# Optimization experiments

Hardware: AMD Instinct MI355X
Metric: run time of the kernel (lower is better)

## Reference

```python
import jax, jax.numpy as jnp
import numpy as np

B, S, V = 1, 4096, 50265
D, H, DH, FF, L = 768, 12, 64, 3072, 12
W = 256  # one-sided window (longformer-base attention_window=512)
EPS = 1e-5
NEG = -1e9


def _ln(x, s, b):
    mu = jnp.mean(x, -1, keepdims=True)
    var = jnp.mean(jnp.square(x - mu), -1, keepdims=True)
    return (x - mu) * jax.lax.rsqrt(var + EPS) * s + b


def _sliding_attn(q, k, v, key_mask):
    # q,k,v: [B,H,S,DH]; key_mask: [B,S] (1 = attend). Banded attention |i-j| <= W.
    b, h, s, dh = q.shape
    c = W
    nc = s // c
    idx = jnp.arange(nc)[:, None] * c + jnp.arange(3 * c)[None, :]  # index into padded key axis
    kp = jnp.pad(k, ((0, 0), (0, 0), (c, c), (0, 0)))
    vp = jnp.pad(v, ((0, 0), (0, 0), (c, c), (0, 0)))
    k3 = kp[:, :, idx]  # [B,H,nc,3c,DH]
    v3 = vp[:, :, idx]
    qc = q.reshape(b, h, nc, c, dh)
    scores = jnp.einsum('bhncd,bhnmd->bhncm', qc, k3) * (1.0 / (dh ** 0.5))
    rel = jnp.arange(3 * c)[None, :] - c - jnp.arange(c)[:, None]  # key_pos - query_pos, [c,3c]
    band = jnp.abs(rel) <= W
    km = jnp.pad(key_mask.astype(bool), ((0, 0), (c, c)))[:, idx]  # [B,nc,3c]
    valid = band[None, None, None] & km[:, None, :, None, :]
    probs = jax.nn.softmax(jnp.where(valid, scores, NEG), axis=-1)
    out = jnp.einsum('bhncm,bhnmd->bhncd', probs, v3)
    return out.reshape(b, h, s, dh)


def _forward(input_ids, attention_mask, word_emb, pos_emb, emb_ln_s, emb_ln_b,
             Wq, bq, Wk, bk, Wv, bv, Wo, bo, ln1_s, ln1_b,
             W1, b1, W2, b2, ln2_s, ln2_b,
             h1w, h1b, h2w, h2b, h3w, h3b):
    b, s = input_ids.shape
    pos = jnp.arange(s) + 2  # roberta-style position offset (padding_idx=1)
    x = word_emb[input_ids] + pos_emb[pos][None]
    x = _ln(x, emb_ln_s, emb_ln_b)
    key_mask = attention_mask

    def block(xc, p):
        wq, bq_, wk, bk_, wv, bv_, wo, bo_, l1s, l1b, w1, b1_, w2, b2_, l2s, l2b = p
        q = (xc @ wq + bq_).reshape(b, s, H, DH).transpose(0, 2, 1, 3)
        k = (xc @ wk + bk_).reshape(b, s, H, DH).transpose(0, 2, 1, 3)
        v = (xc @ wv + bv_).reshape(b, s, H, DH).transpose(0, 2, 1, 3)
        a = _sliding_attn(q, k, v, key_mask).transpose(0, 2, 1, 3).reshape(b, s, D)
        xc = _ln(xc + a @ wo + bo_, l1s, l1b)
        hdd = jax.nn.gelu(xc @ w1 + b1_, approximate=False)
        xc = _ln(xc + hdd @ w2 + b2_, l2s, l2b)
        return xc, None

    x, _ = jax.lax.scan(block, x, (Wq, bq, Wk, bk, Wv, bv, Wo, bo,
                                   ln1_s, ln1_b, W1, b1, W2, b2, ln2_s, ln2_b))

    # gather hidden state at last occurrence of token id 2 (</s>) per row
    eq = (input_ids == 2).astype(jnp.int32)
    sep = s - 1 - jnp.argmax(eq[:, ::-1], axis=1)
    emb = x[jnp.arange(b), sep]  # [B, D]

    z = jax.nn.relu(emb @ h1w + h1b)
    z = jax.nn.relu(z @ h2w + h2b)
    return jnp.tanh(z @ h3w + h3b)  # [B, 1]


def setup_inputs() -> dict:
    key = jax.random.key(0)
    ks = jax.random.split(key, 24)
    sc = 0.02

    def n(k, shape):
        return jax.random.normal(k, shape, jnp.float32) * sc

    input_ids = jax.random.randint(ks[0], (B, S), 0, V)
    input_ids = input_ids.at[:, -1].set(2)  # guarantee a </s> token (id 2)
    attention_mask = jnp.ones((B, S), jnp.int32)
    return {
        'input_ids': input_ids,
        'attention_mask': attention_mask,
        'word_emb': n(ks[1], (V, D)),
        'pos_emb': n(ks[2], (S + 2, D)),
        'emb_ln_s': jnp.ones((D,), jnp.float32),
        'emb_ln_b': jnp.zeros((D,), jnp.float32),
        'Wq': n(ks[3], (L, D, D)), 'bq': jnp.zeros((L, D), jnp.float32),
        'Wk': n(ks[4], (L, D, D)), 'bk': jnp.zeros((L, D), jnp.float32),
        'Wv': n(ks[5], (L, D, D)), 'bv': jnp.zeros((L, D), jnp.float32),
        'Wo': n(ks[6], (L, D, D)), 'bo': jnp.zeros((L, D), jnp.float32),
        'ln1_s': jnp.ones((L, D), jnp.float32), 'ln1_b': jnp.zeros((L, D), jnp.float32),
        'W1': n(ks[7], (L, D, FF)), 'b1': jnp.zeros((L, FF), jnp.float32),
        'W2': n(ks[8], (L, FF, D)), 'b2': jnp.zeros((L, D), jnp.float32),
        'ln2_s': jnp.ones((L, D), jnp.float32), 'ln2_b': jnp.zeros((L, D), jnp.float32),
        'h1w': n(ks[9], (D, 512)), 'h1b': jnp.zeros((512,), jnp.float32),
        'h2w': n(ks[10], (512, 256)), 'h2b': jnp.zeros((256,), jnp.float32),
        'h3w': n(ks[11], (256, 1)), 'h3b': jnp.zeros((1,), jnp.float32),
    }


def reference(input_ids, attention_mask, word_emb, pos_emb, emb_ln_s, emb_ln_b,
              Wq, bq, Wk, bk, Wv, bv, Wo, bo, ln1_s, ln1_b,
              W1, b1, W2, b2, ln2_s, ln2_b,
              h1w, h1b, h2w, h2b, h3w, h3b):
    return _forward(input_ids, attention_mask, word_emb, pos_emb, emb_ln_s, emb_ln_b,
                    Wq, bq, Wk, bk, Wv, bv, Wo, bo, ln1_s, ln1_b,
                    W1, b1, W2, b2, ln2_s, ln2_b,
                    h1w, h1b, h2w, h2b, h3w, h3b)
```

## Files before the change

### kernel.cpp

```cpp
#include <hip/hip_runtime.h>
#include <math.h>

#define S_LEN 4096
#define DMODEL 768
#define NHEAD 12
#define DHEAD 64
#define FFDIM 3072
#define NLAYER 12
#define WIN 256
#define QKVN 2304

typedef __bf16 bf16x8 __attribute__((ext_vector_type(8)));
typedef unsigned short u16x8 __attribute__((ext_vector_type(8)));
typedef unsigned short u16x4 __attribute__((ext_vector_type(4)));
typedef float f32x4 __attribute__((ext_vector_type(4)));

__device__ inline unsigned short f2bf(float f) {
    unsigned int u = __float_as_uint(f);
    u += 0x7fff + ((u >> 16) & 1);
    return (unsigned short)(u >> 16);
}

__device__ inline void gload16(const void* g, void* l) {
    __builtin_amdgcn_global_load_lds((const __attribute__((address_space(1))) void*)g,
                                     (__attribute__((address_space(3))) void*)l, 16, 0, 0);
}

__global__ __launch_bounds__(256) void ln_kernel(const float* __restrict__ in,
                                                 const float* __restrict__ s,
                                                 const float* __restrict__ b,
                                                 float* __restrict__ out,
                                                 unsigned short* __restrict__ outb) {
    const int wv = threadIdx.x >> 6, lane = threadIdx.x & 63;
    const int row = blockIdx.x * 4 + wv;
    const float* p = in + (size_t)row * DMODEL;
    const int c = lane * 4;
    float4 v0 = *(const float4*)&p[c];
    float4 v1 = *(const float4*)&p[c + 256];
    float4 v2 = *(const float4*)&p[c + 512];
    float sum = v0.x + v0.y + v0.z + v0.w + v1.x + v1.y + v1.z + v1.w
              + v2.x + v2.y + v2.z + v2.w;
    float sq  = v0.x*v0.x + v0.y*v0.y + v0.z*v0.z + v0.w*v0.w
              + v1.x*v1.x + v1.y*v1.y + v1.z*v1.z + v1.w*v1.w
              + v2.x*v2.x + v2.y*v2.y + v2.z*v2.z + v2.w*v2.w;
    #pragma unroll
    for (int off = 32; off; off >>= 1) {
        sum += __shfl_xor(sum, off);
        sq  += __shfl_xor(sq, off);
    }
    const float mu = sum * (1.0f / DMODEL);
    const float var = sq * (1.0f / DMODEL) - mu * mu;
    const float rs = rsqrtf(var + 1e-5f);
    float* o = out + (size_t)row * DMODEL;
    unsigned short* ob = outb + (size_t)row * DMODEL;
    #pragma unroll
    for (int seg = 0; seg < 3; ++seg) {
        const int cc = c + seg * 256;
        float4 v = (seg == 0) ? v0 : (seg == 1) ? v1 : v2;
        float4 sv = *(const float4*)&s[cc];
        float4 bv = *(const float4*)&b[cc];
        float4 r;
        r.x = (v.x - mu) * rs * sv.x + bv.x;
        r.y = (v.y - mu) * rs * sv.y + bv.y;
        r.z = (v.z - mu) * rs * sv.z + bv.z;
        r.w = (v.w - mu) * rs * sv.w + bv.w;
        *(float4*)&o[cc] = r;
        u16x4 pk;
        pk[0] = f2bf(r.x); pk[1] = f2bf(r.y); pk[2] = f2bf(r.z); pk[3] = f2bf(r.w);
        *(u16x4*)&ob[cc] = pk;
    }
}

__device__ inline void block_reduce2(float& sum, float& sq) {
    #pragma unroll
    for (int off = 32; off; off >>= 1) {
        sum += __shfl_xor(sum, off);
        sq  += __shfl_xor(sq, off);
    }
    __shared__ float red[8];
    int wid = threadIdx.x >> 6, lane = threadIdx.x & 63;
    if (lane == 0) { red[wid] = sum; red[wid + 4] = sq; }
    __syncthreads();
    sum = red[0] + red[1] + red[2] + red[3];
    sq  = red[4] + red[5] + red[6] + red[7];
    __syncthreads();
}

__global__ __launch_bounds__(256) void embed_ln_kernel(const int* __restrict__ ids,
                                                       const float* __restrict__ wemb,
                                                       const float* __restrict__ pemb,
                                                       const float* __restrict__ s,
                                                       const float* __restrict__ b,
                                                       float* __restrict__ out,
                                                       unsigned short* __restrict__ outb) {
    int row = blockIdx.x, tid = threadIdx.x;
    int id = ids[row];
    const float* wp = wemb + (size_t)id * DMODEL;
    const float* pp = pemb + (size_t)(row + 2) * DMODEL;
    float v0 = wp[tid] + pp[tid];
    float v1 = wp[tid + 256] + pp[tid + 256];
    float v2 = wp[tid + 512] + pp[tid + 512];
    float sum = v0 + v1 + v2;
    float sq  = v0 * v0 + v1 * v1 + v2 * v2;
    block_reduce2(sum, sq);
    float mu = sum * (1.0f / DMODEL);
    float var = sq * (1.0f / DMODEL) - mu * mu;
    float rs = rsqrtf(var + 1e-5f);
    float* o = out + (size_t)row * DMODEL;
    unsigned short* ob = outb + (size_t)row * DMODEL;
    float r0 = (v0 - mu) * rs * s[tid]       + b[tid];
    float r1 = (v1 - mu) * rs * s[tid + 256] + b[tid + 256];
    float r2 = (v2 - mu) * rs * s[tid + 512] + b[tid + 512];
    o[tid] = r0; o[tid + 256] = r1; o[tid + 512] = r2;
    ob[tid] = f2bf(r0); ob[tid + 256] = f2bf(r1); ob[tid + 512] = f2bf(r2);
}

__global__ __launch_bounds__(256) void transpose_all(const float* __restrict__ wq,
                                                     const float* __restrict__ wk,
                                                     const float* __restrict__ wv,
                                                     const float* __restrict__ wo,
                                                     const float* __restrict__ w1,
                                                     const float* __restrict__ w2,
                                                     unsigned short* __restrict__ dq,
                                                     unsigned short* __restrict__ dk,
                                                     unsigned short* __restrict__ dv,
                                                     unsigned short* __restrict__ dwo,
                                                     unsigned short* __restrict__ d1,
                                                     unsigned short* __restrict__ d2) {
    const int id = blockIdx.x;
    const float* src; unsigned short* dst; int C, R, bx, by;
    if (id < 2304) {
        const int m = id / 576, t2 = id % 576;
        src = (m == 0) ? wq : (m == 1) ? wk : (m == 2) ? wv : wo;
        dst = (m == 0) ? dq : (m == 1) ? dk : (m == 2) ? dv : dwo;
        R = 768; C = 768; bx = (t2 % 24) * 32; by = (t2 / 24) * 32;
    } else if (id < 4608) {
        const int t2 = id - 2304;
        src = w1; dst = d1; R = 768; C = 3072;
        bx = (t2 % 96) * 32; by = (t2 / 96) * 32;
    } else {
        const int t2 = id - 4608;
        src = w2; dst = d2; R = 3072; C = 768;
        bx = (t2 % 24) * 32; by = (t2 / 24) * 32;
    }
    __shared__ float tile[32][33];
    const int t = threadIdx.x;
    const int lrow = t >> 3;
    const int lcol = (t & 7) * 4;
    float4 v = *(const float4*)&src[(size_t)(by + lrow) * C + bx + lcol];
    tile[lrow][lcol]     = v.x;
    tile[lrow][lcol + 1] = v.y;
    tile[lrow][lcol + 2] = v.z;
    tile[lrow][lcol + 3] = v.w;
    __syncthreads();
    const int c  = t >> 3;
    const int rp = t & 7;
    unsigned int b0 = f2bf(tile[4 * rp][c]);
    unsigned int b1 = f2bf(tile[4 * rp + 1][c]);
    unsigned int b2 = f2bf(tile[4 * rp + 2][c]);
    unsigned int b3 = f2bf(tile[4 * rp + 3][c]);
    uint2 pk;
    pk.x = (b1 << 16) | b0;
    pk.y = (b3 << 16) | b2;
    *(uint2*)&dst[(size_t)(bx + c) * R + by + 4 * rp] = pk;
}

__global__ __launch_bounds__(256) void bias_concat(const float* __restrict__ bq,
                                                   const float* __restrict__ bk,
                                                   const float* __restrict__ bv,
                                                   float* __restrict__ out) {
    int l = blockIdx.x, t = threadIdx.x;
    for (int i = t; i < DMODEL; i += 256) {
        out[(size_t)l * QKVN + i]              = bq[(size_t)l * DMODEL + i];
        out[(size_t)l * QKVN + DMODEL + i]     = bk[(size_t)l * DMODEL + i];
        out[(size_t)l * QKVN + 2 * DMODEL + i] = bv[(size_t)l * DMODEL + i];
    }
}

template<int MODE, int BN>
__global__ __launch_bounds__(256) void mfma_gemm(const unsigned short* __restrict__ A,
                                                 const unsigned short* __restrict__ Bt,
                                                 const float* __restrict__ bias,
                                                 const float* __restrict__ res,
                                                 void* __restrict__ Cout,
                                                 int M, int N, int K) {
    constexpr int MR = (BN == 128) ? 4 : 2;
    __shared__ unsigned short As[128 * 64];
    __shared__ unsigned short Bs[BN * 64];
    const int tid = threadIdx.x;
    const int wv = tid >> 6, lane = tid & 63;
    const int bm = blockIdx.x * 128, bn = blockIdx.y * BN;
    const int wr = (BN == 128) ? (wv >> 1) * 64 : wv * 32;
    const int wc = (BN == 128) ? (wv & 1) * 64 : 0;
    const int l15 = lane & 15, g = lane >> 4;

    f32x4 acc[MR][4];
    #pragma unroll
    for (int m = 0; m < MR; ++m)
        #pragma unroll
        for (int n = 0; n < 4; ++n)
            #pragma unroll
            for (int e = 0; e < 4; ++e) acc[m][n][e] = 0.f;

    const int srow = tid >> 3;
    const int scol = (tid & 7) * 8;

    for (int k0 = 0; k0 < K; k0 += 64) {
        __syncthreads();
        #pragma unroll
        for (int c = 0; c < 4; ++c)
            gload16(A + (size_t)(bm + c * 32 + srow) * K + k0 + scol,
                    (char*)As + c * 4096 + wv * 1024);
        #pragma unroll
        for (int c = 0; c < BN / 32; ++c)
            gload16(Bt + (size_t)(bn + c * 32 + srow) * K + k0 + scol,
                    (char*)Bs + c * 4096 + wv * 1024);
        __syncthreads();
        #pragma unroll
        for (int kk = 0; kk < 2; ++kk) {
            bf16x8 af[MR], bfr[4];
            #pragma unroll
            for (int m = 0; m < MR; ++m)
                af[m] = *(const bf16x8*)(As + (wr + m * 16 + l15) * 64 + kk * 32 + g * 8);
            #pragma unroll
            for (int n = 0; n < 4; ++n)
                bfr[n] = *(const bf16x8*)(Bs + (wc + n * 16 + l15) * 64 + kk * 32 + g * 8);
            #pragma unroll
            for (int m = 0; m < MR; ++m)
                #pragma unroll
                for (int n = 0; n < 4; ++n)
                    acc[m][n] = __builtin_amdgcn_mfma_f32_16x16x32_bf16(af[m], bfr[n], acc[m][n], 0, 0, 0);
        }
    }

    #pragma unroll
    for (int m = 0; m < MR; ++m) {
        const int row0 = bm + wr + m * 16 + g * 4;
        #pragma unroll
        for (int n = 0; n < 4; ++n) {
            const int col = bn + wc + n * 16 + l15;
            const float bb = bias[col];
            #pragma unroll
            for (int r = 0; r < 4; ++r) {
                float v = acc[m][n][r] + bb;
                if (MODE == 0) {
                    v += res[(size_t)(row0 + r) * N + col];
                    ((float*)Cout)[(size_t)(row0 + r) * N + col] = v;
                } else if (MODE == 1) {
                    ((unsigned short*)Cout)[(size_t)(row0 + r) * N + col] = f2bf(v);
                } else {
                    float gv = 0.5f * v * (1.0f + erff(v * 0.70710678118654752f));
                    ((unsigned short*)Cout)[(size_t)(row0 + r) * N + col] = f2bf(gv);
                }
            }
        }
    }
}

__global__ __launch_bounds__(256) void attn_mfma(const unsigned short* __restrict__ qkv,
                                                 const int* __restrict__ msk,
                                                 unsigned short* __restrict__ aout) {
    __shared__ unsigned short Ks[64 * 64];
    __shared__ unsigned short Vt[64 * 64];
    __shared__ unsigned short Ps[4][16 * 64];
    const int tid = threadIdx.x;
    const int wv = tid >> 6, lane = tid & 63;
    const int l15 = lane & 15, g = lane >> 4;
    const int h = blockIdx.y;
    const int q0 = blockIdx.x * 64;

    const int qrow = q0 + wv * 16 + l15;
    bf16x8 qf[2];
    #pragma unroll
    for (int kk = 0; kk < 2; ++kk)
        qf[kk] = *(const bf16x8*)(qkv + (size_t)qrow * QKVN + h * 64 + kk * 32 + g * 8);

    f32x4 o[4];
    #pragma unroll
    for (int n = 0; n < 4; ++n)
        #pragma unroll
        for (int e = 0; e < 4; ++e) o[n][e] = 0.f;
    float mst[4] = {-3e38f, -3e38f, -3e38f, -3e38f};
    float lst[4] = {0.f, 0.f, 0.f, 0.f};

    const int srow = tid >> 3;
    const int scol = (tid & 7) * 8;
    const int xr  = (l15 & 7) << 3;
    const int kg4 = (tid >> 4) * 4;
    const int dg4 = (tid & 15) * 4;

    for (int c = 0; c < 9; ++c) {
        const int kc = q0 - 256 + c * 64;
        __syncthreads();
        #pragma unroll
        for (int cc = 0; cc < 2; ++cc) {
            const int r = cc * 32 + srow;
            int krow = min(max(kc + r, 0), S_LEN - 1);
            gload16(qkv + (size_t)krow * QKVN + DMODEL + h * 64 + (scol ^ ((r & 7) << 3)),
                    (char*)Ks + cc * 4096 + wv * 1024);
        }
        {
            u16x4 vr[4];
            #pragma unroll
            for (int j = 0; j < 4; ++j) {
                int vrow = min(max(kc + kg4 + j, 0), S_LEN - 1);
                vr[j] = *(const u16x4*)(qkv + (size_t)vrow * QKVN + 2 * DMODEL + h * 64 + dg4);
            }
            #pragma unroll
            for (int i = 0; i < 4; ++i) {
                const int d = dg4 + i;
                const int f = ((d >> 3) ^ d) & 7;
                u16x4 w;
                w[0] = vr[0][i]; w[1] = vr[1][i]; w[2] = vr[2][i]; w[3] = vr[3][i];
                *(u16x4*)(Vt + d * 64 + (kg4 ^ (f << 3))) = w;
            }
        }
        __syncthreads();

        f32x4 s[4];
        #pragma unroll
        for (int n = 0; n < 4; ++n)
            #pragma unroll
            for (int e = 0; e < 4; ++e) s[n][e] = 0.f;
        #pragma unroll
        for (int kk = 0; kk < 2; ++kk) {
            #pragma unroll
            for (int n = 0; n < 4; ++n) {
                bf16x8 kf = *(const bf16x8*)(Ks + (n * 16 + l15) * 64 + ((kk * 32 + g * 8) ^ xr));
                s[n] = __builtin_amdgcn_mfma_f32_16x16x32_bf16(qf[kk], kf, s[n], 0, 0, 0);
            }
        }

        float pv[4][4];
        const int qbase = q0 + wv * 16 + g * 4;
        #pragma unroll
        for (int n = 0; n < 4; ++n) {
            const int key = kc + n * 16 + l15;
            const bool kin = (key >= 0) && (key < S_LEN);
            const int mv = kin ? msk[key] : 0;
            #pragma unroll
            for (int r = 0; r < 4; ++r) {
                const int qa = qbase + r;
                const bool valid = (mv != 0) && (abs(key - qa) <= WIN);
                pv[n][r] = valid ? s[n][r] * 0.125f : -1e9f;
            }
        }
        float scold[4];
        #pragma unroll
        for (int r = 0; r < 4; ++r) {
            float mx = fmaxf(fmaxf(pv[0][r], pv[1][r]), fmaxf(pv[2][r], pv[3][r]));
            mx = fmaxf(mx, __shfl_xor(mx, 1));
            mx = fmaxf(mx, __shfl_xor(mx, 2));
            mx = fmaxf(mx, __shfl_xor(mx, 4));
            mx = fmaxf(mx, __shfl_xor(mx, 8));
            const float nm = fmaxf(mst[r], mx);
            scold[r] = expf(mst[r] - nm);
            float sum = 0.f;
            #pragma unroll
            for (int n = 0; n < 4; ++n) { pv[n][r] = expf(pv[n][r] - nm); sum += pv[n][r]; }
            sum += __shfl_xor(sum, 1); sum += __shfl_xor(sum, 2);
            sum += __shfl_xor(sum, 4); sum += __shfl_xor(sum, 8);
            lst[r] = lst[r] * scold[r] + sum;
            mst[r] = nm;
        }
        #pragma unroll
        for (int n = 0; n < 4; ++n)
            #pragma unroll
            for (int r = 0; r < 4; ++r)
                o[n][r] *= scold[r];

        #pragma unroll
        for (int n = 0; n < 4; ++n)
            #pragma unroll
            for (int r = 0; r < 4; ++r) {
                const int ql = g * 4 + r;
                Ps[wv][ql * 64 + ((n * 16 + l15) ^ ((ql & 7) << 3))] = f2bf(pv[n][r]);
            }

        #pragma unroll
        for (int kk = 0; kk < 2; ++kk) {
            bf16x8 pf = *(const bf16x8*)(Ps[wv] + l15 * 64 + ((kk * 32 + g * 8) ^ xr));
            #pragma unroll
            for (int nd = 0; nd < 4; ++nd) {
                const int d = nd * 16 + l15;
                const int xv = (((nd * 2 + (l15 >> 3)) & 7) ^ (l15 & 7)) << 3;
                bf16x8 vf = *(const bf16x8*)(Vt + d * 64 + ((kk * 32 + g * 8) ^ xv));
                o[nd] = __builtin_amdgcn_mfma_f32_16x16x32_bf16(pf, vf, o[nd], 0, 0, 0);
            }
        }
    }

    #pragma unroll
    for (int r = 0; r < 4; ++r) {
        const float inv = 1.0f / lst[r];
        const int qa = q0 + wv * 16 + g * 4 + r;
        #pragma unroll
        for (int nd = 0; nd < 4; ++nd)
            aout[(size_t)qa * DMODEL + h * 64 + nd * 16 + l15] = f2bf(o[nd][r] * inv);
    }
}

__global__ __launch_bounds__(256) void head1_kernel(const int* __restrict__ ids,
                                                    const float* __restrict__ x,
                                                    const float* __restrict__ w1,
                                                    const float* __restrict__ b1,
                                                    float* __restrict__ z1) {
    const int tid = threadIdx.x;
    __shared__ int sred[256];
    int loc = -1;
    for (int i = tid; i < S_LEN; i += 256)
        if (ids[i] == 2) loc = i;
    sred[tid] = loc;
    __syncthreads();
    for (int s2 = 128; s2; s2 >>= 1) {
        if (tid < s2) sred[tid] = max(sred[tid], sred[tid + s2]);
        __syncthreads();
    }
    const int sep = sred[0] < 0 ? (S_LEN - 1) : sred[0];

    __shared__ float emb[DMODEL];
    for (int d = tid; d < DMODEL; d += 256) emb[d] = x[(size_t)sep * DMODEL + d];
    __syncthreads();

    const int o = blockIdx.x * 64 + (tid & 63);
    const int chunk = tid >> 6;
    float s = 0.f;
    const int d0 = chunk * 192;
    for (int d = d0; d < d0 + 192; ++d)
        s += emb[d] * w1[(size_t)d * 512 + o];
    __shared__ float part[4][64];
    part[chunk][tid & 63] = s;
    __syncthreads();
    if (chunk == 0) {
        float v = part[0][tid] + part[1][tid] + part[2][tid] + part[3][tid] + b1[o];
        z1[o] = fmaxf(v, 0.f);
    }
}

__global__ __launch_bounds__(256) void head2_kernel(const float* __restrict__ z1,
                                                    const float* __restrict__ w2,
                                                    const float* __restrict__ b2,
                                                    const float* __restrict__ w3,
                                                    const float* __restrict__ b3,
                                                    float* __restrict__ out) {
    const int tid = threadIdx.x;
    __shared__ float z1s[512];
    for (int i = tid; i < 512; i += 256) z1s[i] = z1[i];
    __syncthreads();
    float s = b2[tid];
    for (int d = 0; d < 512; ++d) s += z1s[d] * w2[(size_t)d * 256 + tid];
    float z2 = fmaxf(s, 0.f);
    __shared__ float fred[256];
    fred[tid] = z2 * w3[tid];
    __syncthreads();
    for (int s2 = 128; s2; s2 >>= 1) {
        if (tid < s2) fred[tid] += fred[tid + s2];
        __syncthreads();
    }
    if (tid == 0) out[0] = tanhf(fred[0] + b3[0]);
}


extern "C" void kernel_launch(void* const* d_in, const int* in_sizes, int n_in,
                              void* d_out, int out_size, void* d_ws, size_t ws_size,
                              hipStream_t stream) {
    const int*   ids      = (const int*)d_in[0];
    const int*   amask    = (const int*)d_in[1];
    const float* word_emb = (const float*)d_in[2];
    const float* pos_emb  = (const float*)d_in[3];
    const float* emb_s    = (const float*)d_in[4];
    const float* emb_b    = (const float*)d_in[5];
    const float* Wq = (const float*)d_in[6];
    const float* bq = (const float*)d_in[7];
    const float* Wk = (const float*)d_in[8];
    const float* bk = (const float*)d_in[9];
    const float* Wv = (const float*)d_in[10];
    const float* bv = (const float*)d_in[11];
    const float* Wo = (const float*)d_in[12];
    const float* bo = (const float*)d_in[13];
    const float* l1s = (const float*)d_in[14];
    const float* l1b = (const float*)d_in[15];
    const float* W1 = (const float*)d_in[16];
    const float* b1 = (const float*)d_in[17];
    const float* W2 = (const float*)d_in[18];
    const float* b2 = (const float*)d_in[19];
    const float* l2s = (const float*)d_in[20];
    const float* l2b = (const float*)d_in[21];
    const float* h1w = (const float*)d_in[22];
    const float* h1b = (const float*)d_in[23];
    const float* h2w = (const float*)d_in[24];
    const float* h2b = (const float*)d_in[25];
    const float* h3w = (const float*)d_in[26];
    const float* h3b = (const float*)d_in[27];

    char* ws = (char*)d_ws;
    float* x          = (float*)(ws);
    float* t          = (float*)(ws + 12582912);
    unsigned short* xb   = (unsigned short*)(ws + 25165824);
    unsigned short* qkv  = (unsigned short*)(ws + 31457280);
    unsigned short* a    = (unsigned short*)(ws + 50331648);
    unsigned short* hb   = (unsigned short*)(ws + 56623104);
    unsigned short* WqkvT= (unsigned short*)(ws + 81788928);
    unsigned short* WoT  = (unsigned short*)(ws + 85327872);
    unsigned short* W1T  = (unsigned short*)(ws + 86507520);
    unsigned short* W2T  = (unsigned short*)(ws + 91226112);
    float* biascat       = (float*)(ws + 95944704);
    float* z1ws          = (float*)(ws + 96055296);

    bias_concat<<<NLAYER, 256, 0, stream>>>(bq, bk, bv, biascat);
    embed_ln_kernel<<<S_LEN, 256, 0, stream>>>(ids, word_emb, pos_emb, emb_s, emb_b, x, xb);

    const size_t dd = (size_t)DMODEL * DMODEL;
    const size_t df = (size_t)DMODEL * FFDIM;

    for (int l = 0; l < NLAYER; ++l) {
        transpose_all<<<6912, 256, 0, stream>>>(Wq + l * dd, Wk + l * dd, Wv + l * dd, Wo + l * dd,
                                                W1 + l * df, W2 + l * df,
                                                WqkvT, WqkvT + dd, WqkvT + 2 * dd, WoT, W1T, W2T);

        mfma_gemm<1, 128><<<dim3(32, 18), 256, 0, stream>>>(xb, WqkvT, biascat + (size_t)l * QKVN,
                                                            nullptr, qkv, S_LEN, QKVN, DMODEL);
        attn_mfma<<<dim3(S_LEN / 64, NHEAD), 256, 0, stream>>>(qkv, amask, a);

        mfma_gemm<0, 64><<<dim3(32, 12), 256, 0, stream>>>(a, WoT, bo + (size_t)l * DMODEL,
                                                           x, t, S_LEN, DMODEL, DMODEL);
        ln_kernel<<<S_LEN / 4, 256, 0, stream>>>(t, l1s + (size_t)l * DMODEL, l1b + (size_t)l * DMODEL, x, xb);

        mfma_gemm<2, 128><<<dim3(32, 24), 256, 0, stream>>>(xb, W1T, b1 + (size_t)l * FFDIM,
                                                            nullptr, hb, S_LEN, FFDIM, DMODEL);
        mfma_gemm<0, 64><<<dim3(32, 12), 256, 0, stream>>>(hb, W2T, b2 + (size_t)l * DMODEL,
                                                           x, t, S_LEN, DMODEL, FFDIM);
        ln_kernel<<<S_LEN / 4, 256, 0, stream>>>(t, l2s + (size_t)l * DMODEL, l2b + (size_t)l * DMODEL, x, xb);
    }

    head1_kernel<<<8, 256, 0, stream>>>(ids, x, h1w, h1b, z1ws);
    head2_kernel<<<1, 256, 0, stream>>>(z1ws, h2w, h2b, h3w, h3b, (float*)d_out);
}
```

Before: 2.755 ms.

## Split-K the N=768 GEMMs and fuse partial reduction, bias, residual into LayerNorm

```diff
diff --git a/kernel.cpp b/kernel.cpp
--- a/kernel.cpp
+++ b/kernel.cpp
@@ -68,6 +68,62 @@
         u16x4 pk;
         pk[0] = f2bf(r.x); pk[1] = f2bf(r.y); pk[2] = f2bf(r.z); pk[3] = f2bf(r.w);
         *(u16x4*)&ob[cc] = pk;
+    }
+}
+
+__global__ __launch_bounds__(256) void ln2_kernel(const float* __restrict__ p1,
+                                                  const float* __restrict__ p2,
+                                                  const float* __restrict__ bias,
+                                                  const float* __restrict__ xres,
+                                                  const float* __restrict__ s,
+                                                  const float* __restrict__ b,
+                                                  float* __restrict__ outx,
+                                                  unsigned short* __restrict__ outxb) {
+    const int wv = threadIdx.x >> 6, lane = threadIdx.x & 63;
+    const int row = blockIdx.x * 4 + wv;
+    const size_t ro = (size_t)row * DMODEL;
+    const int c = lane * 4;
+    float4 vv[3];
+    float sum = 0.f, sq = 0.f;
+    #pragma unroll
+    for (int seg = 0; seg < 3; ++seg) {
+        const int cc = c + seg * 256;
+        float4 a1 = *(const float4*)&p1[ro + cc];
+        float4 a2 = *(const float4*)&p2[ro + cc];
+        float4 bb = *(const float4*)&bias[cc];
+        float4 xr = *(const float4*)&xres[ro + cc];
+        float4 v;
+        v.x = a1.x + a2.x + bb.x + xr.x;
+        v.y = a1.y + a2.y + bb.y + xr.y;
+        v.z = a1.z + a2.z + bb.z + xr.z;
+        v.w = a1.w + a2.w + bb.w + xr.w;
+        vv[seg] = v;
+        sum += v.x + v.y + v.z + v.w;
+        sq  += v.x*v.x + v.y*v.y + v.z*v.z + v.w*v.w;
+    }
+    #pragma unroll
+    for (int off = 32; off; off >>= 1) {
+        sum += __shfl_xor(sum, off);
+        sq  += __shfl_xor(sq, off);
+    }
+    const float mu = sum * (1.0f / DMODEL);
+    const float var = sq * (1.0f / DMODEL) - mu * mu;
+    const float rs = rsqrtf(var + 1e-5f);
+    #pragma unroll
+    for (int seg = 0; seg < 3; ++seg) {
+        const int cc = c + seg * 256;
+        float4 v = vv[seg];
+        float4 sv = *(const float4*)&s[cc];
+        float4 bv = *(const float4*)&b[cc];
+        float4 r;
+        r.x = (v.x - mu) * rs * sv.x + bv.x;
+        r.y = (v.y - mu) * rs * sv.y + bv.y;
+        r.z = (v.z - mu) * rs * sv.z + bv.z;
+        r.w = (v.w - mu) * rs * sv.w + bv.w;
+        *(float4*)&outx[ro + cc] = r;
+        u16x4 pk;
+        pk[0] = f2bf(r.x); pk[1] = f2bf(r.y); pk[2] = f2bf(r.z); pk[3] = f2bf(r.w);
+        *(u16x4*)&outxb[ro + cc] = pk;
     }
 }
 
@@ -181,15 +237,15 @@
 __global__ __launch_bounds__(256) void mfma_gemm(const unsigned short* __restrict__ A,
                                                  const unsigned short* __restrict__ Bt,
                                                  const float* __restrict__ bias,
-                                                 const float* __restrict__ res,
                                                  void* __restrict__ Cout,
-                                                 int M, int N, int K) {
+                                                 int M, int N, int K, int Kstride) {
     constexpr int MR = (BN == 128) ? 4 : 2;
     __shared__ unsigned short As[128 * 64];
     __shared__ unsigned short Bs[BN * 64];
     const int tid = threadIdx.x;
     const int wv = tid >> 6, lane = tid & 63;
     const int bm = blockIdx.x * 128, bn = blockIdx.y * BN;
+    const size_t kbase = (size_t)blockIdx.z * K;
     const int wr = (BN == 128) ? (wv >> 1) * 64 : wv * 32;
     const int wc = (BN == 128) ? (wv & 1) * 64 : 0;
     const int l15 = lane & 15, g = lane >> 4;
@@ -209,11 +265,11 @@
         __syncthreads();
         #pragma unroll
         for (int c = 0; c < 4; ++c)
-            gload16(A + (size_t)(bm + c * 32 + srow) * K + k0 + scol,
+            gload16(A + (size_t)(bm + c * 32 + srow) * Kstride + kbase + k0 + scol,
                     (char*)As + c * 4096 + wv * 1024);
         #pragma unroll
         for (int c = 0; c < BN / 32; ++c)
-            gload16(Bt + (size_t)(bn + c * 32 + srow) * K + k0 + scol,
+            gload16(Bt + (size_t)(bn + c * 32 + srow) * Kstride + kbase + k0 + scol,
                     (char*)Bs + c * 4096 + wv * 1024);
         __syncthreads();
         #pragma unroll
@@ -233,24 +289,28 @@
         }
     }
 
+    const size_t zoff = (MODE == 3) ? (size_t)blockIdx.z * M * N : 0;
     #pragma unroll
     for (int m = 0; m < MR; ++m) {
         const int row0 = bm + wr + m * 16 + g * 4;
         #pragma unroll
         for (int n = 0; n < 4; ++n) {
             const int col = bn + wc + n * 16 + l15;
-            const float bb = bias[col];
-            #pragma unroll
-            for (int r = 0; r < 4; ++r) {
-                float v = acc[m][n][r] + bb;
-                if (MODE == 0) {
-                    v += res[(size_t)(row0 + r) * N + col];
-                    ((float*)Cout)[(size_t)(row0 + r) * N + col] = v;
-                } else if (MODE == 1) {
-                    ((unsigned short*)Cout)[(size_t)(row0 + r) * N + col] = f2bf(v);
-                } else {
-                    float gv = 0.5f * v * (1.0f + erff(v * 0.70710678118654752f));
-                    ((unsigned short*)Cout)[(size_t)(row0 + r) * N + col] = f2bf(gv);
+            if (MODE == 3) {
+                #pragma unroll
+                for (int r = 0; r < 4; ++r)
+                    ((float*)Cout)[zoff + (size_t)(row0 + r) * N + col] = acc[m][n][r];
+            } else {
+                const float bb = bias[col];
+                #pragma unroll
+                for (int r = 0; r < 4; ++r) {
+                    float v = acc[m][n][r] + bb;
+                    if (MODE == 1) {
+                        ((unsigned short*)Cout)[(size_t)(row0 + r) * N + col] = f2bf(v);
+                    } else {
+                        float gv = 0.5f * v * (1.0f + erff(v * 0.70710678118654752f));
+                        ((unsigned short*)Cout)[(size_t)(row0 + r) * N + col] = f2bf(gv);
+                    }
                 }
             }
         }
@@ -495,7 +555,7 @@
 
     char* ws = (char*)d_ws;
     float* x          = (float*)(ws);
-    float* t          = (float*)(ws + 12582912);
+    float* p1         = (float*)(ws + 12582912);
     unsigned short* xb   = (unsigned short*)(ws + 25165824);
     unsigned short* qkv  = (unsigned short*)(ws + 31457280);
     unsigned short* a    = (unsigned short*)(ws + 50331648);
@@ -506,6 +566,11 @@
     unsigned short* W2T  = (unsigned short*)(ws + 91226112);
     float* biascat       = (float*)(ws + 95944704);
     float* z1ws          = (float*)(ws + 96055296);
+    float* p2            = (float*)(ws + 100663296);
+
+    float* p12 = p1;
+    p12 = p2;
+    float* p12b = p12 + (size_t)S_LEN * DMODEL;
 
     bias_concat<<<NLAYER, 256, 0, stream>>>(bq, bk, bv, biascat);
     embed_ln_kernel<<<S_LEN, 256, 0, stream>>>(ids, word_emb, pos_emb, emb_s, emb_b, x, xb);
@@ -519,18 +584,22 @@
                                                 WqkvT, WqkvT + dd, WqkvT + 2 * dd, WoT, W1T, W2T);
 
         mfma_gemm<1, 128><<<dim3(32, 18), 256, 0, stream>>>(xb, WqkvT, biascat + (size_t)l * QKVN,
-                                                            nullptr, qkv, S_LEN, QKVN, DMODEL);
+                                                            qkv, S_LEN, QKVN, DMODEL, DMODEL);
         attn_mfma<<<dim3(S_LEN / 64, NHEAD), 256, 0, stream>>>(qkv, amask, a);
 
-        mfma_gemm<0, 64><<<dim3(32, 12), 256, 0, stream>>>(a, WoT, bo + (size_t)l * DMODEL,
-                                                           x, t, S_LEN, DMODEL, DMODEL);
-        ln_kernel<<<S_LEN / 4, 256, 0, stream>>>(t, l1s + (size_t)l * DMODEL, l1b + (size_t)l * DMODEL, x, xb);
+        mfma_gemm<3, 128><<<dim3(32, 6, 2), 256, 0, stream>>>(a, WoT, nullptr,
+                                                              p12, S_LEN, DMODEL, 384, DMODEL);
+        ln2_kernel<<<S_LEN / 4, 256, 0, stream>>>(p12, p12b, bo + (size_t)l * DMODEL, x,
+                                                  l1s + (size_t)l * DMODEL, l1b + (size_t)l * DMODEL,
+                                                  x, xb);
 
         mfma_gemm<2, 128><<<dim3(32, 24), 256, 0, stream>>>(xb, W1T, b1 + (size_t)l * FFDIM,
-                                                            nullptr, hb, S_LEN, FFDIM, DMODEL);
-        mfma_gemm<0, 64><<<dim3(32, 12), 256, 0, stream>>>(hb, W2T, b2 + (size_t)l * DMODEL,
-                                                           x, t, S_LEN, DMODEL, FFDIM);
-        ln_kernel<<<S_LEN / 4, 256, 0, stream>>>(t, l2s + (size_t)l * DMODEL, l2b + (size_t)l * DMODEL, x, xb);
+                                                            hb, S_LEN, FFDIM, DMODEL, DMODEL);
+        mfma_gemm<3, 128><<<dim3(32, 6, 2), 256, 0, stream>>>(hb, W2T, nullptr,
+                                                              p12, S_LEN, DMODEL, 1536, FFDIM);
+        ln2_kernel<<<S_LEN / 4, 256, 0, stream>>>(p12, p12b, b2 + (size_t)l * DMODEL, x,
+                                                  l2s + (size_t)l * DMODEL, l2b + (size_t)l * DMODEL,
+                                                  x, xb);
     }
 
     head1_kernel<<<8, 256, 0, stream>>>(ids, x, h1w, h1b, z1ws);
```

Result: faster. 2.585 ms (-6.1%).
